# Kernel tuning notes

Hardware: AMD Instinct MI355X
Metric: run time of the kernel (lower is better)

Reference implementation:

```python
import jax, jax.numpy as jnp
import numpy as np

N_HEAD, D_HEAD, D_MODEL = 16, 64, 1024
QLEN, MLEN, BSZ = 512, 512, 8
KLEN = QLEN + MLEN
SCALE = 1.0 / D_HEAD ** 0.5
LN_EPS = 1e-5


def rel_shift(x):
    # x: [qlen, klen, bsz, n_head] -- Transformer-XL pad/reshape shift trick
    q, k, b, n = x.shape
    x_pad = jnp.pad(x, ((0, 0), (1, 0), (0, 0), (0, 0)))
    x_pad = x_pad.reshape(k + 1, q, b, n)
    return x_pad[1:].reshape(q, k, b, n)


def setup_inputs() -> dict:
    key = jax.random.key(0)
    ks = jax.random.split(key, 10)
    s = 0.02
    return {
        'w': jax.random.normal(ks[0], (QLEN, BSZ, D_MODEL), jnp.float32),
        'r': jax.random.normal(ks[1], (KLEN, D_MODEL), jnp.float32),
        'mems': jax.random.normal(ks[2], (MLEN, BSZ, D_MODEL), jnp.float32),
        'r_w_bias': jax.random.normal(ks[3], (N_HEAD, D_HEAD), jnp.float32) * s,
        'r_r_bias': jax.random.normal(ks[4], (N_HEAD, D_HEAD), jnp.float32) * s,
        'Wq': jax.random.normal(ks[5], (N_HEAD * D_HEAD, D_MODEL), jnp.float32) * s,
        'Wkv': jax.random.normal(ks[6], (2 * N_HEAD * D_HEAD, D_MODEL), jnp.float32) * s,
        'Wr': jax.random.normal(ks[7], (N_HEAD * D_HEAD, D_MODEL), jnp.float32) * s,
        'br': jnp.zeros((N_HEAD * D_HEAD,), jnp.float32),
        'Wo': jax.random.normal(ks[8], (D_MODEL, N_HEAD * D_HEAD), jnp.float32) * s,
        'bo': jnp.zeros((D_MODEL,), jnp.float32),
        'gamma': jnp.ones((D_MODEL,), jnp.float32),
        'beta': jnp.zeros((D_MODEL,), jnp.float32),
    }


def reference(w, r, mems, r_w_bias, r_r_bias, Wq, Wkv, Wr, br, Wo, bo, gamma, beta):
    qlen, bsz, _ = w.shape
    cat = jnp.concatenate([mems, w], axis=0)           # [klen, b, d]
    klen = cat.shape[0]
    mlen = klen - qlen

    q = (w @ Wq.T).reshape(qlen, bsz, N_HEAD, D_HEAD)   # [i, b, n, d]
    kv = (cat @ Wkv.T).reshape(klen, bsz, N_HEAD, 2 * D_HEAD)
    k, v = kv[..., :D_HEAD], kv[..., D_HEAD:]           # [j, b, n, d]
    rk = (r @ Wr.T + br).reshape(klen, N_HEAD, D_HEAD)  # [j, n, d]

    AC = jnp.einsum('ibnd,jbnd->ijbn', q + r_w_bias, k)
    BD = jnp.einsum('ibnd,jnd->ijbn', q + r_r_bias, rk)
    BD = rel_shift(BD)
    score = (AC + BD) * SCALE                           # [i, j, b, n]

    # causal mask with memory: query i attends to keys j <= i + mlen
    i_idx = jnp.arange(qlen)[:, None]
    j_idx = jnp.arange(klen)[None, :]
    mask = j_idx > (i_idx + mlen)
    score = jnp.where(mask[:, :, None, None], -1e30, score)

    prob = jax.nn.softmax(score, axis=1)
    attn_vec = jnp.einsum('ijbn,jbnd->ibnd', prob, v).reshape(qlen, bsz, N_HEAD * D_HEAD)
    attn_out = attn_vec @ Wo.T + bo

    # IdentityResidualGate: x + relu(y), then LayerNorm
    y = w + jax.nn.relu(attn_out)
    mu = jnp.mean(y, axis=-1, keepdims=True)
    var = jnp.mean(jnp.square(y - mu), axis=-1, keepdims=True)
    return (y - mu) * jax.lax.rsqrt(var + LN_EPS) * gamma + beta
```

## Files before the change

kernel.cpp:

```cpp
#include <hip/hip_runtime.h>
#include <hip/hip_bf16.h>
#include <cstdint>
#include <cstddef>

typedef __attribute__((ext_vector_type(4))) float f32x4;
typedef __attribute__((ext_vector_type(8))) short bf16x8;
using u16 = unsigned short;

#define ATT_SCALE 0.125f

__device__ __forceinline__ u16 f2b(float f) {
    union { float f; uint32_t u; } x; x.f = f;
    uint32_t r = x.u + 0x7fffu + ((x.u >> 16) & 1u);
    return (u16)(r >> 16);
}

#define GLDS16(g, s)                                                        \
    __builtin_amdgcn_global_load_lds(                                       \
        (const __attribute__((address_space(1))) uint32_t*)(g),             \
        (__attribute__((address_space(3))) uint32_t*)(s), 16, 0, 0)

__global__ __launch_bounds__(256) void prep_kernel(
    const float* __restrict__ mems, const float* __restrict__ w,
    const float* __restrict__ r, const float* __restrict__ Wq,
    const float* __restrict__ Wkv, const float* __restrict__ Wr,
    const float* __restrict__ Wo, u16* __restrict__ cat_b,
    u16* __restrict__ r_b, u16* __restrict__ Wq_b, u16* __restrict__ Wkv_b,
    u16* __restrict__ Wr_b, u16* __restrict__ Wo_b) {
    int bid = blockIdx.x;
    if (bid < 8192) {
        int col4 = threadIdx.x;
        float4 v;
        int b, oj;
        if (bid < 4096) {
            v = reinterpret_cast<const float4*>(mems)[(size_t)bid * 256 + col4];
            b = bid & 7; oj = bid >> 3;
        } else {
            int rrow = bid - 4096;
            v = reinterpret_cast<const float4*>(w)[(size_t)rrow * 256 + col4];
            b = rrow & 7; oj = 512 + (rrow >> 3);
        }
        uint2 o;
        o.x = (uint32_t)f2b(v.x) | ((uint32_t)f2b(v.y) << 16);
        o.y = (uint32_t)f2b(v.z) | ((uint32_t)f2b(v.w) << 16);
        reinterpret_cast<uint2*>(cat_b)[(size_t)(b * 1024 + oj) * 256 + col4] = o;
        return;
    }
    bid -= 8192;
    const float4* src;
    uint2* dst;
    if (bid < 1024)      { src = (const float4*)r;   dst = (uint2*)r_b; }
    else if (bid < 2048) { src = (const float4*)Wq;  dst = (uint2*)Wq_b;  bid -= 1024; }
    else if (bid < 4096) { src = (const float4*)Wkv; dst = (uint2*)Wkv_b; bid -= 2048; }
    else if (bid < 5120) { src = (const float4*)Wr;  dst = (uint2*)Wr_b;  bid -= 4096; }
    else                 { src = (const float4*)Wo;  dst = (uint2*)Wo_b;  bid -= 5120; }
    int idx = bid * 256 + threadIdx.x;
    float4 v = src[idx];
    uint2 o;
    o.x = (uint32_t)f2b(v.x) | ((uint32_t)f2b(v.y) << 16);
    o.y = (uint32_t)f2b(v.z) | ((uint32_t)f2b(v.w) << 16);
    dst[idx] = o;
}

__global__ __launch_bounds__(512, 1) void kv_gemm(const u16* __restrict__ catb,
                                                  const u16* __restrict__ Wkvb,
                                                  u16* __restrict__ kb,
                                                  u16* __restrict__ vtb) {
    __shared__ u16 sA[2][256][64];
    __shared__ u16 sB[2][256][64];
    const int tid = threadIdx.x;
    const int wid = tid >> 6, lane = tid & 63;
    const int lr = lane & 15, lg = lane >> 4;
    const int bm = blockIdx.x * 256, bn = blockIdx.y * 256;
    const int Wm = (wid >> 2) * 128, Wn = (wid & 3) * 64;
    const int srow = tid >> 3, scol = tid & 7;
    const int xs = lr & 7;
    const u16* A = catb + (size_t)bm * 1024;
    const u16* B = Wkvb + (size_t)bn * 1024;
    f32x4 acc[8][4] = {};

#pragma unroll
    for (int p = 0; p < 4; p++) {
        int row = p * 64 + srow;
        int cs = (scol ^ (row & 7)) * 8;
        GLDS16(A + (size_t)row * 1024 + cs, &sA[0][row][scol * 8]);
        GLDS16(B + (size_t)row * 1024 + cs, &sB[0][row][scol * 8]);
    }
    __syncthreads();

    int cur = 0;
    for (int t = 0; t < 16; t++) {
        if (t < 15) {
            const int k0n = (t + 1) * 64;
#pragma unroll
            for (int p = 0; p < 4; p++) {
                int row = p * 64 + srow;
                int cs = (scol ^ (row & 7)) * 8;
                GLDS16(A + (size_t)row * 1024 + k0n + cs, &sA[cur ^ 1][row][scol * 8]);
                GLDS16(B + (size_t)row * 1024 + k0n + cs, &sB[cur ^ 1][row][scol * 8]);
            }
        }
#pragma unroll
        for (int ks = 0; ks < 2; ks++) {
            bf16x8 af[8], bfr[4];
#pragma unroll
            for (int mi = 0; mi < 8; mi++)
                af[mi] = *reinterpret_cast<const bf16x8*>(
                    &sA[cur][Wm + mi * 16 + lr][((ks * 4 + lg) ^ xs) * 8]);
#pragma unroll
            for (int ni = 0; ni < 4; ni++)
                bfr[ni] = *reinterpret_cast<const bf16x8*>(
                    &sB[cur][Wn + ni * 16 + lr][((ks * 4 + lg) ^ xs) * 8]);
#pragma unroll
            for (int mi = 0; mi < 8; mi++)
#pragma unroll
                for (int ni = 0; ni < 4; ni++)
                    acc[mi][ni] = __builtin_amdgcn_mfma_f32_16x16x32_bf16(
                        af[mi], bfr[ni], acc[mi][ni], 0, 0, 0);
        }
        __syncthreads();
        cur ^= 1;
    }
#pragma unroll
    for (int mi = 0; mi < 8; mi++)
#pragma unroll
        for (int ni = 0; ni < 4; ni++) {
            const int m0 = bm + Wm + mi * 16 + lg * 4;
            const int c = bn + Wn + ni * 16 + lr;
            const int b = m0 >> 10, j0 = m0 & 1023;
            const int n = c >> 7, dd = c & 127;
            if (dd < 64) {
#pragma unroll
                for (int rr = 0; rr < 4; rr++)
                    kb[(((size_t)(b * 16 + n)) * 1024 + j0 + rr) * 64 + dd] =
                        f2b(acc[mi][ni][rr]);
            } else {
                uint2 pk;
                pk.x = (uint32_t)f2b(acc[mi][ni][0]) | ((uint32_t)f2b(acc[mi][ni][1]) << 16);
                pk.y = (uint32_t)f2b(acc[mi][ni][2]) | ((uint32_t)f2b(acc[mi][ni][3]) << 16);
                *reinterpret_cast<uint2*>(
                    vtb + (((size_t)(b * 16 + n)) * 64 + (dd - 64)) * 1024 + j0) = pk;
            }
        }
}

__global__ __launch_bounds__(256) void qr_gemm(
    const u16* __restrict__ catb, const u16* __restrict__ Wqb,
    const u16* __restrict__ rb, const u16* __restrict__ Wrb,
    const float* __restrict__ bw, const float* __restrict__ brr,
    const float* __restrict__ br, u16* __restrict__ qwb,
    u16* __restrict__ qrb, u16* __restrict__ rkb) {
    __shared__ uint4 sA[128][8];
    __shared__ uint4 sB[128][8];
    const int idx = blockIdx.x;
    const u16 *A, *B;
    int bx, by, epi;
    if (idx < 256) {
        epi = 0; B = Wqb; bx = idx & 31; by = idx >> 5;
        int bm0 = bx * 128;
        A = catb + ((size_t)(bm0 >> 9) * 1024 + 512 + (bm0 & 511)) * 1024;
    } else {
        epi = 2; B = Wrb;
        int l = idx - 256; bx = l & 7; by = l >> 3;
        A = rb + (size_t)bx * 128 * 1024;
    }
    const int tid = threadIdx.x;
    const int wid = tid >> 6, lane = tid & 63;
    const int lr = lane & 15, lg = lane >> 4;
    const int bm = bx * 128, bn = by * 128;
    const int wm = (wid >> 1) * 64, wn = (wid & 1) * 64;
    const int srow = tid >> 3, scol = tid & 7;
    f32x4 acc[4][4] = {};

    for (int k0 = 0; k0 < 1024; k0 += 64) {
#pragma unroll
        for (int p = 0; p < 4; p++) {
            int row = p * 32 + srow;
            GLDS16(A + (size_t)row * 1024 + k0 + scol * 8, &sA[row][scol]);
            GLDS16(B + (size_t)(bn + row) * 1024 + k0 + scol * 8, &sB[row][scol]);
        }
        __syncthreads();
#pragma unroll
        for (int ks = 0; ks < 2; ks++) {
            bf16x8 af[4], bfr[4];
#pragma unroll
            for (int x = 0; x < 4; x++) {
                af[x] = *reinterpret_cast<const bf16x8*>(&sA[wm + x * 16 + lr][ks * 4 + lg]);
                bfr[x] = *reinterpret_cast<const bf16x8*>(&sB[wn + x * 16 + lr][ks * 4 + lg]);
            }
#pragma unroll
            for (int mi = 0; mi < 4; mi++)
#pragma unroll
                for (int ni = 0; ni < 4; ni++)
                    acc[mi][ni] = __builtin_amdgcn_mfma_f32_16x16x32_bf16(
                        af[mi], bfr[ni], acc[mi][ni], 0, 0, 0);
        }
        __syncthreads();
    }
#pragma unroll
    for (int mi = 0; mi < 4; mi++)
#pragma unroll
        for (int ni = 0; ni < 4; ni++) {
            const int m0 = bm + wm + mi * 16 + lg * 4;
            const int c = bn + wn + ni * 16 + lr;
            if (epi == 0) {
#pragma unroll
                for (int rr = 0; rr < 4; rr++) {
                    int m = m0 + rr;
                    qwb[(size_t)m * 1024 + c] = f2b(acc[mi][ni][rr] + bw[c]);
                    qrb[(size_t)m * 1024 + c] = f2b(acc[mi][ni][rr] + brr[c]);
                }
            } else {
                const int nh = c >> 6, d = c & 63;
#pragma unroll
                for (int rr = 0; rr < 4; rr++)
                    rkb[((size_t)nh * 1024 + m0 + rr) * 64 + d] = f2b(acc[mi][ni][rr] + br[c]);
            }
        }
}

__global__ __launch_bounds__(256) void gemm_out(const u16* __restrict__ A,
                                                const u16* __restrict__ B,
                                                const float* __restrict__ wres,
                                                const float* __restrict__ bo,
                                                float* __restrict__ y) {
    __shared__ uint4 sA[128][8];
    __shared__ uint4 sB[128][8];
    const int tid = threadIdx.x;
    const int wid = tid >> 6, lane = tid & 63;
    const int lr = lane & 15, lg = lane >> 4;
    const int bm = blockIdx.x * 128, bn = blockIdx.y * 128;
    const int wm = (wid >> 1) * 64, wn = (wid & 1) * 64;
    const int srow = tid >> 3, scol = tid & 7;
    f32x4 acc[4][4] = {};

    for (int k0 = 0; k0 < 1024; k0 += 64) {
#pragma unroll
        for (int p = 0; p < 4; p++) {
            int row = p * 32 + srow;
            GLDS16(A + (size_t)(bm + row) * 1024 + k0 + scol * 8, &sA[row][scol]);
            GLDS16(B + (size_t)(bn + row) * 1024 + k0 + scol * 8, &sB[row][scol]);
        }
        __syncthreads();
#pragma unroll
        for (int ks = 0; ks < 2; ks++) {
            bf16x8 af[4], bfr[4];
#pragma unroll
            for (int x = 0; x < 4; x++) {
                af[x] = *reinterpret_cast<const bf16x8*>(&sA[wm + x * 16 + lr][ks * 4 + lg]);
                bfr[x] = *reinterpret_cast<const bf16x8*>(&sB[wn + x * 16 + lr][ks * 4 + lg]);
            }
#pragma unroll
            for (int mi = 0; mi < 4; mi++)
#pragma unroll
                for (int ni = 0; ni < 4; ni++)
                    acc[mi][ni] = __builtin_amdgcn_mfma_f32_16x16x32_bf16(
                        af[mi], bfr[ni], acc[mi][ni], 0, 0, 0);
        }
        __syncthreads();
    }
#pragma unroll
    for (int mi = 0; mi < 4; mi++)
#pragma unroll
        for (int ni = 0; ni < 4; ni++)
#pragma unroll
            for (int rr = 0; rr < 4; rr++) {
                int m = bm + wm + mi * 16 + lg * 4 + rr;
                int c = bn + wn + ni * 16 + lr;
                y[(size_t)m * 1024 + c] =
                    wres[(size_t)m * 1024 + c] + fmaxf(acc[mi][ni][rr] + bo[c], 0.0f);
            }
}

__global__ __launch_bounds__(256, 2) void attn_kernel(const u16* __restrict__ qw,
                                                      const u16* __restrict__ qr,
                                                      const u16* __restrict__ kbuf,
                                                      const u16* __restrict__ vt,
                                                      const u16* __restrict__ rkb,
                                                      u16* __restrict__ attnv) {
    __shared__ uint4 ksh[64][8];
    __shared__ uint4 vsh[64][8];
    __shared__ uint4 rsh[128][8];
    __shared__ float bds[4][16][82];
    __shared__ u16 ps[4][16][72];
    const int bid = blockIdx.x;
    const int wg = (bid & 7) * 128 + (bid >> 3);
    const int i0 = (wg & 7) * 64;
    const int bnid = wg >> 3;
    const int b = bnid & 7, n = bnid >> 3;
    const int tid = threadIdx.x, wid = tid >> 6, lane = tid & 63;
    const int lr = lane & 15, lg = lane >> 4;
    const int it = i0 + wid * 16;

    const u16* qwp = qw + ((size_t)(b * 512 + it + lr)) * 1024 + n * 64;
    const u16* qrp = qr + ((size_t)(b * 512 + it + lr)) * 1024 + n * 64;
    bf16x8 aqw[2], aqr[2];
#pragma unroll
    for (int ks = 0; ks < 2; ks++) {
        aqw[ks] = *reinterpret_cast<const bf16x8*>(qwp + (ks * 4 + lg) * 8);
        aqr[ks] = *reinterpret_cast<const bf16x8*>(qrp + (ks * 4 + lg) * 8);
    }
    const u16* kp = kbuf + ((size_t)(b * 16 + n)) * 65536;
    const u16* vp = vt + ((size_t)(b * 16 + n)) * 65536;
    const u16* rp = rkb + (size_t)n * 65536;

    f32x4 acc[4] = {};
    float lpart[4] = {0.f, 0.f, 0.f, 0.f};
    const int xs = lr & 7;
    const int rbase = 48 - 16 * wid;

    const int nt = (i0 + 639) >> 6;
    for (int t = 0; t < nt; t++) {
        const int j0 = t << 6;
        const int jrb = j0 + 448 - i0;
#pragma unroll
        for (int inst = 0; inst < 2; inst++) {
            int gi = wid * 128 + inst * 64 + lane;
            int row = gi >> 3, c = gi & 7;
            int cs = (c ^ (row & 7)) * 8;
            GLDS16(kp + (size_t)(j0 + row) * 64 + cs,
                   (char*)ksh + (size_t)(wid * 128 + inst * 64) * 16);
            GLDS16(vp + (size_t)row * 1024 + j0 + cs,
                   (char*)vsh + (size_t)(wid * 128 + inst * 64) * 16);
        }
#pragma unroll
        for (int inst = 0; inst < 4; inst++) {
            int gi = wid * 256 + inst * 64 + lane;
            int row = gi >> 3, c = gi & 7;
            int grow = jrb + row;
            if (grow > 1023) grow = 1023;
            GLDS16(rp + (size_t)grow * 64 + (c ^ (row & 7)) * 8,
                   (char*)rsh + (size_t)(wid * 256 + inst * 64) * 16);
        }
        __syncthreads();

        f32x4 s[4] = {};
#pragma unroll
        for (int fj = 0; fj < 4; fj++)
#pragma unroll
            for (int ks = 0; ks < 2; ks++) {
                bf16x8 bk = *reinterpret_cast<const bf16x8*>(
                    &ksh[fj * 16 + lr][(ks * 4 + lg) ^ xs]);
                s[fj] = __builtin_amdgcn_mfma_f32_16x16x32_bf16(aqw[ks], bk, s[fj], 0, 0, 0);
            }
        f32x4 bd[5] = {};
#pragma unroll
        for (int fb = 0; fb < 5; fb++) {
            int rel = rbase + fb * 16 + lr;
#pragma unroll
            for (int ks = 0; ks < 2; ks++) {
                bf16x8 brk = *reinterpret_cast<const bf16x8*>(
                    &rsh[rel][(ks * 4 + lg) ^ xs]);
                bd[fb] = __builtin_amdgcn_mfma_f32_16x16x32_bf16(aqr[ks], brk, bd[fb], 0, 0, 0);
            }
        }
#pragma unroll
        for (int fb = 0; fb < 5; fb++)
#pragma unroll
            for (int rr = 0; rr < 4; rr++)
                bds[wid][lg * 4 + rr][fb * 16 + lr] = bd[fb][rr];

#pragma unroll
        for (int fj = 0; fj < 4; fj++)
#pragma unroll
            for (int rr = 0; rr < 4; rr++) {
                const int di = lg * 4 + rr;
                float v = (s[fj][rr] + bds[wid][di][fj * 16 + lr + 15 - di]) * ATT_SCALE;
                float e = (j0 + fj * 16 + lr <= it + di + 512) ? __expf(v) : 0.0f;
                lpart[rr] += e;
                ps[wid][di][fj * 16 + lr] = f2b(e);
            }
#pragma unroll
        for (int kc = 0; kc < 2; kc++) {
            bf16x8 ap = *reinterpret_cast<const bf16x8*>(&ps[wid][lr][kc * 32 + lg * 8]);
#pragma unroll
            for (int nd = 0; nd < 4; nd++) {
                bf16x8 bv = *reinterpret_cast<const bf16x8*>(
                    &vsh[nd * 16 + lr][(kc * 4 + lg) ^ xs]);
                acc[nd] = __builtin_amdgcn_mfma_f32_16x16x32_bf16(ap, bv, acc[nd], 0, 0, 0);
            }
        }
        __syncthreads();
    }
    float l[4];
#pragma unroll
    for (int rr = 0; rr < 4; rr++) {
        float x = lpart[rr];
        x += __shfl_xor(x, 1);
        x += __shfl_xor(x, 2);
        x += __shfl_xor(x, 4);
        x += __shfl_xor(x, 8);
        l[rr] = x;
    }
#pragma unroll
    for (int nd = 0; nd < 4; nd++)
#pragma unroll
        for (int rr = 0; rr < 4; rr++) {
            int i = it + lg * 4 + rr;
            int d = nd * 16 + lr;
            attnv[((size_t)i * 8 + b) * 1024 + n * 64 + d] = f2b(acc[nd][rr] / l[rr]);
        }
}

__global__ __launch_bounds__(256) void ln_kernel(const float* __restrict__ y,
                                                 const float* __restrict__ gamma,
                                                 const float* __restrict__ beta,
                                                 float* __restrict__ out) {
    __shared__ float rs[8];
    int row = blockIdx.x, tid = threadIdx.x;
    const float4 v = reinterpret_cast<const float4*>(y + (size_t)row * 1024)[tid];
    float s = v.x + v.y + v.z + v.w;
    float s2 = v.x * v.x + v.y * v.y + v.z * v.z + v.w * v.w;
#pragma unroll
    for (int m = 1; m < 64; m <<= 1) {
        s += __shfl_xor(s, m);
        s2 += __shfl_xor(s2, m);
    }
    if ((tid & 63) == 0) {
        rs[tid >> 6] = s;
        rs[4 + (tid >> 6)] = s2;
    }
    __syncthreads();
    s = rs[0] + rs[1] + rs[2] + rs[3];
    s2 = rs[4] + rs[5] + rs[6] + rs[7];
    float mu = s * (1.0f / 1024.0f);
    float var = s2 * (1.0f / 1024.0f) - mu * mu;
    float inv = rsqrtf(var + 1e-5f);
    float4 g = reinterpret_cast<const float4*>(gamma)[tid];
    float4 be = reinterpret_cast<const float4*>(beta)[tid];
    float4 o;
    o.x = (v.x - mu) * inv * g.x + be.x;
    o.y = (v.y - mu) * inv * g.y + be.y;
    o.z = (v.z - mu) * inv * g.z + be.z;
    o.w = (v.w - mu) * inv * g.w + be.w;
    reinterpret_cast<float4*>(out + (size_t)row * 1024)[tid] = o;
}

extern "C" void kernel_launch(void* const* d_in, const int* in_sizes, int n_in,
                              void* d_out, int out_size, void* d_ws, size_t ws_size,
                              hipStream_t stream) {
    (void)in_sizes; (void)n_in; (void)out_size; (void)ws_size;
    const float* w_in  = (const float*)d_in[0];
    const float* r_in  = (const float*)d_in[1];
    const float* mems  = (const float*)d_in[2];
    const float* bw    = (const float*)d_in[3];
    const float* brr   = (const float*)d_in[4];
    const float* Wq    = (const float*)d_in[5];
    const float* Wkv   = (const float*)d_in[6];
    const float* Wr    = (const float*)d_in[7];
    const float* br    = (const float*)d_in[8];
    const float* Wo    = (const float*)d_in[9];
    const float* bo    = (const float*)d_in[10];
    const float* gamma = (const float*)d_in[11];
    const float* beta  = (const float*)d_in[12];

    char* base = (char*)d_ws;
    size_t off = 0;
    auto alloc = [&](size_t bytes) -> char* {
        char* p = base + off;
        off += (bytes + 255) & ~(size_t)255;
        return p;
    };
    u16* cat_b = (u16*)alloc((size_t)8192 * 1024 * 2);
    u16* r_b   = (u16*)alloc((size_t)1024 * 1024 * 2);
    u16* Wq_b  = (u16*)alloc((size_t)1024 * 1024 * 2);
    u16* Wkv_b = (u16*)alloc((size_t)2048 * 1024 * 2);
    u16* Wr_b  = (u16*)alloc((size_t)1024 * 1024 * 2);
    u16* Wo_b  = (u16*)alloc((size_t)1024 * 1024 * 2);
    u16* qw_b  = (u16*)alloc((size_t)4096 * 1024 * 2);
    u16* qr_b  = (u16*)alloc((size_t)4096 * 1024 * 2);
    u16* k_b   = (u16*)alloc((size_t)128 * 1024 * 64 * 2);
    u16* vt_b  = (u16*)alloc((size_t)128 * 64 * 1024 * 2);
    u16* rk_b  = (u16*)alloc((size_t)16 * 1024 * 64 * 2);
    u16* av_b  = (u16*)alloc((size_t)4096 * 1024 * 2);
    float* y = (float*)cat_b;

    prep_kernel<<<14336, 256, 0, stream>>>(mems, w_in, r_in, Wq, Wkv, Wr, Wo,
                                           cat_b, r_b, Wq_b, Wkv_b, Wr_b, Wo_b);

    kv_gemm<<<dim3(32, 8), 512, 0, stream>>>(cat_b, Wkv_b, k_b, vt_b);
    qr_gemm<<<320, 256, 0, stream>>>(cat_b, Wq_b, r_b, Wr_b, bw, brr, br,
                                     qw_b, qr_b, rk_b);

    attn_kernel<<<1024, 256, 0, stream>>>(qw_b, qr_b, k_b, vt_b, rk_b, av_b);

    gemm_out<<<dim3(32, 8), 256, 0, stream>>>(av_b, Wo_b, w_in, bo, y);

    ln_kernel<<<4096, 256, 0, stream>>>(y, gamma, beta, (float*)d_out);
}
```

Measured before the change: 202.1 us.

## Double-buffer LDS in projection GEMMs and shrink attention BD scratch to bf16

The qr_gemm and gemm_out kernels now keep two LDS stages and issue the global-to-LDS loads for the next K tile before computing on the current one. This overlaps memory latency with MFMA work and drops one barrier per iteration. The attention kernel stores its BD scratch tile as bf16 instead of fp32 and raises its occupancy hint from 2 to 3 blocks per CU, trading some precision in the positional score for lower LDS use. Both GEMMs also get a min-blocks hint of 2.

After: 204.6 us. About the same (+1.2%).

```diff
diff --git a/kernel.cpp b/kernel.cpp
--- a/kernel.cpp
+++ b/kernel.cpp
@@ -13,6 +13,9 @@
     union { float f; uint32_t u; } x; x.f = f;
     uint32_t r = x.u + 0x7fffu + ((x.u >> 16) & 1u);
     return (u16)(r >> 16);
+}
+__device__ __forceinline__ float b2f(u16 u) {
+    union { uint32_t u; float f; } x; x.u = (uint32_t)u << 16; return x.f;
 }
 
 #define GLDS16(g, s)                                                        \
@@ -144,14 +147,14 @@
         }
 }
 
-__global__ __launch_bounds__(256) void qr_gemm(
+__global__ __launch_bounds__(256, 2) void qr_gemm(
     const u16* __restrict__ catb, const u16* __restrict__ Wqb,
     const u16* __restrict__ rb, const u16* __restrict__ Wrb,
     const float* __restrict__ bw, const float* __restrict__ brr,
     const float* __restrict__ br, u16* __restrict__ qwb,
     u16* __restrict__ qrb, u16* __restrict__ rkb) {
-    __shared__ uint4 sA[128][8];
-    __shared__ uint4 sB[128][8];
+    __shared__ u16 sA[2][128][64];
+    __shared__ u16 sB[2][128][64];
     const int idx = blockIdx.x;
     const u16 *A, *B;
     int bx, by, epi;
@@ -172,21 +175,35 @@
     const int srow = tid >> 3, scol = tid & 7;
     f32x4 acc[4][4] = {};
 
-    for (int k0 = 0; k0 < 1024; k0 += 64) {
-#pragma unroll
-        for (int p = 0; p < 4; p++) {
-            int row = p * 32 + srow;
-            GLDS16(A + (size_t)row * 1024 + k0 + scol * 8, &sA[row][scol]);
-            GLDS16(B + (size_t)(bn + row) * 1024 + k0 + scol * 8, &sB[row][scol]);
-        }
-        __syncthreads();
+#pragma unroll
+    for (int p = 0; p < 4; p++) {
+        int row = p * 32 + srow;
+        GLDS16(A + (size_t)row * 1024 + scol * 8, &sA[0][row][scol * 8]);
+        GLDS16(B + (size_t)(bn + row) * 1024 + scol * 8, &sB[0][row][scol * 8]);
+    }
+    __syncthreads();
+
+    int cur = 0;
+    for (int t = 0; t < 16; t++) {
+        if (t < 15) {
+            const int k0n = (t + 1) * 64;
+#pragma unroll
+            for (int p = 0; p < 4; p++) {
+                int row = p * 32 + srow;
+                GLDS16(A + (size_t)row * 1024 + k0n + scol * 8, &sA[cur ^ 1][row][scol * 8]);
+                GLDS16(B + (size_t)(bn + row) * 1024 + k0n + scol * 8,
+                       &sB[cur ^ 1][row][scol * 8]);
+            }
+        }
 #pragma unroll
         for (int ks = 0; ks < 2; ks++) {
             bf16x8 af[4], bfr[4];
 #pragma unroll
             for (int x = 0; x < 4; x++) {
-                af[x] = *reinterpret_cast<const bf16x8*>(&sA[wm + x * 16 + lr][ks * 4 + lg]);
-                bfr[x] = *reinterpret_cast<const bf16x8*>(&sB[wn + x * 16 + lr][ks * 4 + lg]);
+                af[x] = *reinterpret_cast<const bf16x8*>(
+                    &sA[cur][wm + x * 16 + lr][(ks * 4 + lg) * 8]);
+                bfr[x] = *reinterpret_cast<const bf16x8*>(
+                    &sB[cur][wn + x * 16 + lr][(ks * 4 + lg) * 8]);
             }
 #pragma unroll
             for (int mi = 0; mi < 4; mi++)
@@ -196,6 +213,7 @@
                         af[mi], bfr[ni], acc[mi][ni], 0, 0, 0);
         }
         __syncthreads();
+        cur ^= 1;
     }
 #pragma unroll
     for (int mi = 0; mi < 4; mi++)
@@ -219,13 +237,13 @@
         }
 }
 
-__global__ __launch_bounds__(256) void gemm_out(const u16* __restrict__ A,
-                                                const u16* __restrict__ B,
-                                                const float* __restrict__ wres,
-                                                const float* __restrict__ bo,
-                                                float* __restrict__ y) {
-    __shared__ uint4 sA[128][8];
-    __shared__ uint4 sB[128][8];
+__global__ __launch_bounds__(256, 2) void gemm_out(const u16* __restrict__ A,
+                                                   const u16* __restrict__ B,
+                                                   const float* __restrict__ wres,
+                                                   const float* __restrict__ bo,
+                                                   float* __restrict__ y) {
+    __shared__ u16 sA[2][128][64];
+    __shared__ u16 sB[2][128][64];
     const int tid = threadIdx.x;
     const int wid = tid >> 6, lane = tid & 63;
     const int lr = lane & 15, lg = lane >> 4;
@@ -234,21 +252,36 @@
     const int srow = tid >> 3, scol = tid & 7;
     f32x4 acc[4][4] = {};
 
-    for (int k0 = 0; k0 < 1024; k0 += 64) {
-#pragma unroll
-        for (int p = 0; p < 4; p++) {
-            int row = p * 32 + srow;
-            GLDS16(A + (size_t)(bm + row) * 1024 + k0 + scol * 8, &sA[row][scol]);
-            GLDS16(B + (size_t)(bn + row) * 1024 + k0 + scol * 8, &sB[row][scol]);
-        }
-        __syncthreads();
+#pragma unroll
+    for (int p = 0; p < 4; p++) {
+        int row = p * 32 + srow;
+        GLDS16(A + (size_t)(bm + row) * 1024 + scol * 8, &sA[0][row][scol * 8]);
+        GLDS16(B + (size_t)(bn + row) * 1024 + scol * 8, &sB[0][row][scol * 8]);
+    }
+    __syncthreads();
+
+    int cur = 0;
+    for (int t = 0; t < 16; t++) {
+        if (t < 15) {
+            const int k0n = (t + 1) * 64;
+#pragma unroll
+            for (int p = 0; p < 4; p++) {
+                int row = p * 32 + srow;
+                GLDS16(A + (size_t)(bm + row) * 1024 + k0n + scol * 8,
+                       &sA[cur ^ 1][row][scol * 8]);
+                GLDS16(B + (size_t)(bn + row) * 1024 + k0n + scol * 8,
+                       &sB[cur ^ 1][row][scol * 8]);
+            }
+        }
 #pragma unroll
         for (int ks = 0; ks < 2; ks++) {
             bf16x8 af[4], bfr[4];
 #pragma unroll
             for (int x = 0; x < 4; x++) {
-                af[x] = *reinterpret_cast<const bf16x8*>(&sA[wm + x * 16 + lr][ks * 4 + lg]);
-                bfr[x] = *reinterpret_cast<const bf16x8*>(&sB[wn + x * 16 + lr][ks * 4 + lg]);
+                af[x] = *reinterpret_cast<const bf16x8*>(
+                    &sA[cur][wm + x * 16 + lr][(ks * 4 + lg) * 8]);
+                bfr[x] = *reinterpret_cast<const bf16x8*>(
+                    &sB[cur][wn + x * 16 + lr][(ks * 4 + lg) * 8]);
             }
 #pragma unroll
             for (int mi = 0; mi < 4; mi++)
@@ -258,6 +291,7 @@
                         af[mi], bfr[ni], acc[mi][ni], 0, 0, 0);
         }
         __syncthreads();
+        cur ^= 1;
     }
 #pragma unroll
     for (int mi = 0; mi < 4; mi++)
@@ -272,7 +306,7 @@
             }
 }
 
-__global__ __launch_bounds__(256, 2) void attn_kernel(const u16* __restrict__ qw,
+__global__ __launch_bounds__(256, 3) void attn_kernel(const u16* __restrict__ qw,
                                                       const u16* __restrict__ qr,
                                                       const u16* __restrict__ kbuf,
                                                       const u16* __restrict__ vt,
@@ -281,7 +315,7 @@
     __shared__ uint4 ksh[64][8];
     __shared__ uint4 vsh[64][8];
     __shared__ uint4 rsh[128][8];
-    __shared__ float bds[4][16][82];
+    __shared__ u16 bds[4][16][82];
     __shared__ u16 ps[4][16][72];
     const int bid = blockIdx.x;
     const int wg = (bid & 7) * 128 + (bid >> 3);
@@ -358,14 +392,14 @@
         for (int fb = 0; fb < 5; fb++)
 #pragma unroll
             for (int rr = 0; rr < 4; rr++)
-                bds[wid][lg * 4 + rr][fb * 16 + lr] = bd[fb][rr];
+                bds[wid][lg * 4 + rr][fb * 16 + lr] = f2b(bd[fb][rr]);
 
 #pragma unroll
         for (int fj = 0; fj < 4; fj++)
 #pragma unroll
             for (int rr = 0; rr < 4; rr++) {
                 const int di = lg * 4 + rr;
-                float v = (s[fj][rr] + bds[wid][di][fj * 16 + lr + 15 - di]) * ATT_SCALE;
+                float v = (s[fj][rr] + b2f(bds[wid][di][fj * 16 + lr + 15 - di])) * ATT_SCALE;
                 float e = (j0 + fj * 16 + lr <= it + di + 512) ? __expf(v) : 0.0f;
                 lpart[rr] += e;
                 ps[wid][di][fj * 16 + lr] = f2b(e);
```
